# Kernel tuning notes

Measured on AMD Instinct MI355X. Metric: run time of the kernel, lower is better.

## Reference

```python
import jax, jax.numpy as jnp
import numpy as np

B, Q, C = 256, 900, 91


def setup_inputs() -> dict:
    key = jax.random.key(0)
    k1, k2, k3 = jax.random.split(key, 3)
    pred_logits = jax.random.normal(k1, (B, Q, C), dtype=jnp.float32)
    # cxcywh boxes in [0,1] like DETR-style normalized outputs
    pred_boxes = jax.random.uniform(k2, (B, Q, 4), dtype=jnp.float32)
    # original image sizes (h, w) in pixels, roughly COCO-scale
    target_sizes = jax.random.uniform(k3, (B, 2), dtype=jnp.float32) * 1024.0 + 256.0
    return {"pred_logits": pred_logits, "pred_boxes": pred_boxes, "target_sizes": target_sizes}


def reference(pred_logits, pred_boxes, target_sizes):
    # prob over flattened (query, class) pairs; top-k with k = num_queries
    prob = jax.nn.sigmoid(pred_logits).reshape(B, Q * C)
    scores, topk_indexes = jax.lax.top_k(prob, Q)          # [B, Q]
    topk_boxes = topk_indexes // C                          # query index
    labels = topk_indexes % C                               # class index
    # cxcywh -> xyxy
    cx, cy, w, h = jnp.split(pred_boxes, 4, axis=-1)
    boxes = jnp.concatenate([cx - 0.5 * w, cy - 0.5 * h, cx + 0.5 * w, cy + 0.5 * h], axis=-1)  # [B, Q, 4]
    # gather boxes for selected queries
    boxes = jnp.take_along_axis(boxes, topk_boxes[..., None], axis=1)  # [B, Q, 4]
    # scale to absolute image coordinates: target_sizes = (h, w)
    img_h, img_w = target_sizes[:, 0], target_sizes[:, 1]
    scale_fct = jnp.stack([img_w, img_h, img_w, img_h], axis=1)        # [B, 4]
    boxes = boxes * scale_fct[:, None, :]
    return scores, labels, boxes
```

## Files before the change

### kernel.cpp

```cpp
#include <hip/hip_runtime.h>

#define NB 256
#define NQ 900
#define NC 91
#define QC (NQ * NC)
#define NF4 (QC / 4)

#define HBINS 1024
#define PREBIN 320
#define CAP 4096
#define LCAP 1024

#define SLICES 8
#define F4S 2560
#define NTA 256
#define NTC 512

#define CNT_OFF   0
#define HIST_OFF  1024
#define CAND_OFF  (1024 + NB * HBINS * 4)
#define ZERO_BYTES CAND_OFF

__device__ __forceinline__ int bin_of(float x) {
    int b = (int)floorf((x + 8.0f) * 32.0f);
    return max(0, min(HBINS - 1, b));
}

__global__ __launch_bounds__(NTA, 4) void hist_gather(
    const float* __restrict__ logits, unsigned int* __restrict__ g_cnt,
    unsigned int* __restrict__ g_hist, unsigned long long* __restrict__ g_cand) {
    __shared__ unsigned int hist[HBINS];
    __shared__ unsigned long long lc[LCAP];
    __shared__ unsigned int l_cnt;
    __shared__ unsigned int l_base;

    const unsigned int tid = threadIdx.x;
    const unsigned int b = blockIdx.x >> 3;
    const unsigned int s = blockIdx.x & 7;

    for (unsigned int i = tid; i < HBINS; i += NTA) hist[i] = 0;
    if (tid == 0) l_cnt = 0;
    __syncthreads();

    const float4* row = (const float4*)(logits + (size_t)b * QC);
    const unsigned int beg = s * F4S;
    const unsigned int end = min(beg + F4S, (unsigned int)NF4);
    for (unsigned int i = beg + tid; i < end; i += NTA) {
        float4 v = row[i];
        #pragma unroll
        for (int j = 0; j < 4; ++j) {
            float x = (&v.x)[j];
            int bn = bin_of(x);
            atomicAdd(&hist[bn], 1u);
            if (bn >= PREBIN) {
                unsigned int p = atomicAdd(&l_cnt, 1u);
                if (p < LCAP)
                    lc[p] = ((unsigned long long)__float_as_uint(x) << 32) |
                            (unsigned int)(i * 4u + j);
            }
        }
    }
    __syncthreads();

    unsigned int* gh = g_hist + (size_t)b * HBINS;
    for (unsigned int i = tid; i < HBINS; i += NTA) {
        unsigned int h = hist[i];
        if (h) atomicAdd(&gh[i], h);
    }

    unsigned int raw = l_cnt;
    unsigned int n = min(raw, (unsigned int)LCAP);
    if (tid == 0) {
        unsigned int add = n + ((raw > LCAP) ? (unsigned int)(CAP + 1) : 0u);
        l_base = atomicAdd(&g_cnt[b], add);
    }
    __syncthreads();
    const unsigned int base = l_base;
    unsigned long long* gc = g_cand + (size_t)b * CAP;
    for (unsigned int i = tid; i < n; i += NTA) {
        unsigned int p = base + i;
        if (p < CAP) gc[p] = lc[i];
    }
}

__global__ __launch_bounds__(NTC, 1) void select_sort_emit(
    const float* __restrict__ logits, const float* __restrict__ boxes,
    const float* __restrict__ tsz, const unsigned int* __restrict__ g_cnt,
    const unsigned int* __restrict__ g_hist,
    const unsigned long long* __restrict__ g_cand, float* __restrict__ out) {
    __shared__ unsigned int hist[HBINS];
    __shared__ unsigned int csum[NTC];
    __shared__ unsigned long long sbuf[2048];
    __shared__ unsigned int s_cnt;
    __shared__ unsigned int s_b1;

    const unsigned int tid = threadIdx.x;
    const unsigned int b = blockIdx.x;

    const unsigned int* gh = g_hist + (size_t)b * HBINS;
    for (unsigned int i = tid; i < HBINS; i += NTC) hist[i] = gh[i];
    if (tid == 0) s_cnt = 0;
    __syncthreads();

    csum[tid] = hist[2 * tid] + hist[2 * tid + 1];
    __syncthreads();
    for (unsigned int off = 1; off < NTC; off <<= 1) {
        unsigned int v = csum[tid];
        unsigned int a = (tid + off < NTC) ? csum[tid + off] : 0;
        __syncthreads();
        csum[tid] = v + a;
        __syncthreads();
    }
    if (csum[tid] >= NQ && (tid == NTC - 1 || csum[tid + 1] < NQ)) {
        unsigned int running = (tid == NTC - 1) ? 0u : csum[tid + 1];
        unsigned int b1 = 2 * tid;
        for (int bn = 2 * (int)tid + 1; bn >= 2 * (int)tid; --bn) {
            running += hist[bn];
            if (running >= NQ) { b1 = (unsigned int)bn; break; }
        }
        s_b1 = b1;
    }
    __syncthreads();
    const unsigned int b1 = s_b1;
    const unsigned int cnt = g_cnt[b];
    const bool fast = (b1 >= PREBIN) && (cnt <= CAP);

    if (fast) {
        const unsigned long long* gc = g_cand + (size_t)b * CAP;
        for (unsigned int i = tid; i < cnt; i += NTC) {
            unsigned long long kc = gc[i];
            float x = __uint_as_float((unsigned int)(kc >> 32));
            if (bin_of(x) >= (int)b1) {
                unsigned int idx = (unsigned int)kc;
                float p = (float)(1.0 / (1.0 + exp(-(double)x)));
                unsigned int pos = atomicAdd(&s_cnt, 1u);
                if (pos < 2048)
                    sbuf[pos] = ((unsigned long long)__float_as_uint(p) << 32) |
                                (unsigned int)(~idx);
            }
        }
    } else {
        const float4* row = (const float4*)(logits + (size_t)b * QC);
        for (unsigned int i = tid; i < NF4; i += NTC) {
            float4 v = row[i];
            #pragma unroll
            for (int j = 0; j < 4; ++j) {
                float x = (&v.x)[j];
                if (bin_of(x) >= (int)b1) {
                    unsigned int idx = i * 4u + j;
                    float p = (float)(1.0 / (1.0 + exp(-(double)x)));
                    unsigned int pos = atomicAdd(&s_cnt, 1u);
                    if (pos < 2048)
                        sbuf[pos] = ((unsigned long long)__float_as_uint(p) << 32) |
                                    (unsigned int)(~idx);
                }
            }
        }
    }
    __syncthreads();
    const unsigned int n = min(s_cnt, 2048u);
    const unsigned int NS = (n <= 1024u) ? 1024u : 2048u;
    for (unsigned int i = n + tid; i < NS; i += NTC) sbuf[i] = 0ull;

    for (unsigned int k = 2; k <= NS; k <<= 1) {
        for (unsigned int j = k >> 1; j > 0; j >>= 1) {
            __syncthreads();
            for (unsigned int i = tid; i < NS; i += NTC) {
                unsigned int l = i ^ j;
                if (l > i) {
                    unsigned long long a = sbuf[i], c = sbuf[l];
                    bool up = ((i & k) == 0);
                    if (up ? (a < c) : (a > c)) { sbuf[i] = c; sbuf[l] = a; }
                }
            }
        }
    }
    __syncthreads();

    const float img_h = tsz[2 * b];
    const float img_w = tsz[2 * b + 1];
    float* out_scores = out;
    float* out_labels = out + (size_t)NB * NQ;
    float4* out_boxes = (float4*)(out + (size_t)2 * NB * NQ);
    const float4* boxes4 = (const float4*)boxes;

    for (unsigned int r = tid; r < NQ; r += NTC) {
        unsigned long long item = sbuf[r];
        float p = __uint_as_float((unsigned int)(item >> 32));
        unsigned int idx = ~((unsigned int)item);
        unsigned int q = idx / NC;
        unsigned int lab = idx - q * NC;
        float4 bx = boxes4[b * NQ + q];
        float x0 = (bx.x - 0.5f * bx.z) * img_w;
        float y0 = (bx.y - 0.5f * bx.w) * img_h;
        float x1 = (bx.x + 0.5f * bx.z) * img_w;
        float y1 = (bx.y + 0.5f * bx.w) * img_h;
        out_scores[(size_t)b * NQ + r] = p;
        out_labels[(size_t)b * NQ + r] = (float)lab;
        out_boxes[(size_t)b * NQ + r] = make_float4(x0, y0, x1, y1);
    }
}

extern "C" void kernel_launch(void* const* d_in, const int* in_sizes, int n_in,
                              void* d_out, int out_size, void* d_ws, size_t ws_size,
                              hipStream_t stream) {
    const float* logits = (const float*)d_in[0];
    const float* boxes = (const float*)d_in[1];
    const float* tsz = (const float*)d_in[2];
    float* out = (float*)d_out;

    unsigned char* ws = (unsigned char*)d_ws;
    unsigned int* g_cnt = (unsigned int*)(ws + CNT_OFF);
    unsigned int* g_hist = (unsigned int*)(ws + HIST_OFF);
    unsigned long long* g_cand = (unsigned long long*)(ws + CAND_OFF);

    hipMemsetAsync(ws, 0, ZERO_BYTES, stream);
    hist_gather<<<NB * SLICES, NTA, 0, stream>>>(logits, g_cnt, g_hist, g_cand);
    select_sort_emit<<<NB, NTC, 0, stream>>>(logits, boxes, tsz, g_cnt, g_hist,
                                             g_cand, out);
}
```

Before: 55.19 us.

## Store per-slice histograms and candidates to drop global atomics and memset

```diff
diff --git a/kernel.cpp b/kernel.cpp
--- a/kernel.cpp
+++ b/kernel.cpp
@@ -8,18 +8,15 @@
 
 #define HBINS 1024
 #define PREBIN 320
-#define CAP 4096
-#define LCAP 1024
-
 #define SLICES 8
+#define SCAP 512
 #define F4S 2560
 #define NTA 256
 #define NTC 512
 
 #define CNT_OFF   0
-#define HIST_OFF  1024
-#define CAND_OFF  (1024 + NB * HBINS * 4)
-#define ZERO_BYTES CAND_OFF
+#define HIST_OFF  (NB * SLICES * 4)
+#define CAND_OFF  (HIST_OFF + NB * SLICES * HBINS * 4)
 
 __device__ __forceinline__ int bin_of(float x) {
     int b = (int)floorf((x + 8.0f) * 32.0f);
@@ -30,13 +27,13 @@
     const float* __restrict__ logits, unsigned int* __restrict__ g_cnt,
     unsigned int* __restrict__ g_hist, unsigned long long* __restrict__ g_cand) {
     __shared__ unsigned int hist[HBINS];
-    __shared__ unsigned long long lc[LCAP];
+    __shared__ unsigned long long lc[SCAP];
     __shared__ unsigned int l_cnt;
-    __shared__ unsigned int l_base;
 
     const unsigned int tid = threadIdx.x;
     const unsigned int b = blockIdx.x >> 3;
     const unsigned int s = blockIdx.x & 7;
+    const unsigned int sl = blockIdx.x;
 
     for (unsigned int i = tid; i < HBINS; i += NTA) hist[i] = 0;
     if (tid == 0) l_cnt = 0;
@@ -54,7 +51,7 @@
             atomicAdd(&hist[bn], 1u);
             if (bn >= PREBIN) {
                 unsigned int p = atomicAdd(&l_cnt, 1u);
-                if (p < LCAP)
+                if (p < SCAP)
                     lc[p] = ((unsigned long long)__float_as_uint(x) << 32) |
                             (unsigned int)(i * 4u + j);
             }
@@ -62,25 +59,14 @@
     }
     __syncthreads();
 
-    unsigned int* gh = g_hist + (size_t)b * HBINS;
-    for (unsigned int i = tid; i < HBINS; i += NTA) {
-        unsigned int h = hist[i];
-        if (h) atomicAdd(&gh[i], h);
-    }
-
-    unsigned int raw = l_cnt;
-    unsigned int n = min(raw, (unsigned int)LCAP);
-    if (tid == 0) {
-        unsigned int add = n + ((raw > LCAP) ? (unsigned int)(CAP + 1) : 0u);
-        l_base = atomicAdd(&g_cnt[b], add);
-    }
-    __syncthreads();
-    const unsigned int base = l_base;
-    unsigned long long* gc = g_cand + (size_t)b * CAP;
-    for (unsigned int i = tid; i < n; i += NTA) {
-        unsigned int p = base + i;
-        if (p < CAP) gc[p] = lc[i];
-    }
+    unsigned int* gh = g_hist + (size_t)sl * HBINS;
+    for (unsigned int i = tid; i < HBINS; i += NTA) gh[i] = hist[i];
+
+    const unsigned int raw = l_cnt;
+    const unsigned int n = min(raw, (unsigned int)SCAP);
+    unsigned long long* gc = g_cand + (size_t)sl * SCAP;
+    for (unsigned int i = tid; i < n; i += NTA) gc[i] = lc[i];
+    if (tid == 0) g_cnt[sl] = raw;
 }
 
 __global__ __launch_bounds__(NTC, 1) void select_sort_emit(
@@ -93,13 +79,20 @@
     __shared__ unsigned long long sbuf[2048];
     __shared__ unsigned int s_cnt;
     __shared__ unsigned int s_b1;
+    __shared__ unsigned int scnts[SLICES];
 
     const unsigned int tid = threadIdx.x;
     const unsigned int b = blockIdx.x;
 
-    const unsigned int* gh = g_hist + (size_t)b * HBINS;
-    for (unsigned int i = tid; i < HBINS; i += NTC) hist[i] = gh[i];
+    const unsigned int* gh = g_hist + (size_t)b * SLICES * HBINS;
+    for (unsigned int i = tid; i < HBINS; i += NTC) {
+        unsigned int h = 0;
+        #pragma unroll
+        for (int s = 0; s < SLICES; ++s) h += gh[s * HBINS + i];
+        hist[i] = h;
+    }
     if (tid == 0) s_cnt = 0;
+    if (tid < SLICES) scnts[tid] = g_cnt[b * SLICES + tid];
     __syncthreads();
 
     csum[tid] = hist[2 * tid] + hist[2 * tid + 1];
@@ -122,21 +115,26 @@
     }
     __syncthreads();
     const unsigned int b1 = s_b1;
-    const unsigned int cnt = g_cnt[b];
-    const bool fast = (b1 >= PREBIN) && (cnt <= CAP);
+
+    bool fast = (b1 >= PREBIN);
+    for (int s = 0; s < SLICES; ++s) fast = fast && (scnts[s] <= SCAP);
 
     if (fast) {
-        const unsigned long long* gc = g_cand + (size_t)b * CAP;
-        for (unsigned int i = tid; i < cnt; i += NTC) {
-            unsigned long long kc = gc[i];
-            float x = __uint_as_float((unsigned int)(kc >> 32));
-            if (bin_of(x) >= (int)b1) {
-                unsigned int idx = (unsigned int)kc;
-                float p = (float)(1.0 / (1.0 + exp(-(double)x)));
-                unsigned int pos = atomicAdd(&s_cnt, 1u);
-                if (pos < 2048)
-                    sbuf[pos] = ((unsigned long long)__float_as_uint(p) << 32) |
-                                (unsigned int)(~idx);
+        const unsigned long long* gc = g_cand + (size_t)b * SLICES * SCAP;
+        for (unsigned int slot = tid; slot < SLICES * SCAP; slot += NTC) {
+            unsigned int s = slot >> 9;
+            unsigned int i = slot & (SCAP - 1);
+            if (i < scnts[s]) {
+                unsigned long long kc = gc[slot];
+                float x = __uint_as_float((unsigned int)(kc >> 32));
+                if (bin_of(x) >= (int)b1) {
+                    unsigned int idx = (unsigned int)kc;
+                    float p = (float)(1.0 / (1.0 + exp(-(double)x)));
+                    unsigned int pos = atomicAdd(&s_cnt, 1u);
+                    if (pos < 2048)
+                        sbuf[pos] = ((unsigned long long)__float_as_uint(p) << 32) |
+                                    (unsigned int)(~idx);
+                }
             }
         }
     } else {
@@ -214,7 +212,6 @@
     unsigned int* g_hist = (unsigned int*)(ws + HIST_OFF);
     unsigned long long* g_cand = (unsigned long long*)(ws + CAND_OFF);
 
-    hipMemsetAsync(ws, 0, ZERO_BYTES, stream);
     hist_gather<<<NB * SLICES, NTA, 0, stream>>>(logits, g_cnt, g_hist, g_cand);
     select_sort_emit<<<NB, NTC, 0, stream>>>(logits, boxes, tsz, g_cnt, g_hist,
                                              g_cand, out);
```

New measurement: 50.65 us. -8.2%, faster.
